# Performance work log

Hardware: AMD Instinct MI355X
Metric: run time of the kernel (lower is better)

The kernel has to match this reference:

```python
import jax, jax.numpy as jnp
import numpy as np

THRESHOLD = 1e-6
BLOCK_M = 64  # tile size over the batch/row dimension (prescan granularity)


def setup_inputs() -> dict:
    key = jax.random.key(0)
    k_x, k_w, k_b, k_m = jax.random.split(key, 4)
    N, C_IN, C_OUT = 16384, 4096, 4096
    n_tiles = N // BLOCK_M
    x = jax.random.normal(k_x, (N, C_IN), dtype=jnp.float32)
    # which is what the Dynamic-K prescan exploits
    tile_mask = (jax.random.uniform(k_m, (n_tiles, C_IN)) > 0.6).astype(jnp.float32)
    x = (x.reshape(n_tiles, BLOCK_M, C_IN) * tile_mask[:, None, :]).reshape(N, C_IN)
    weight = jax.random.normal(k_w, (C_OUT, C_IN), dtype=jnp.float32) * 0.02
    bias = jax.random.normal(k_b, (C_OUT,), dtype=jnp.float32) * 0.01
    return {"x": x, "weight": weight, "bias": bias}


def reference(x, weight, bias):
    # Tile-level Dynamic-K sparse linear: per tile of BLOCK_M rows, a channel c
    # is active iff max |x[tile, c]| > threshold; only active channels are
    # multiplied/accumulated. Equivalent math: zero inactive channels, then GEMM.
    N, C_IN = x.shape
    n_tiles = N // BLOCK_M
    xt = x.reshape(n_tiles, BLOCK_M, C_IN)
    active = (jnp.max(jnp.abs(xt), axis=1) > THRESHOLD)  # [n_tiles, C_IN]
    xm = xt * active[:, None, :].astype(x.dtype)
    # y[t,b,o] = sum_c xm[t,b,c] * weight[o,c]
    y = jnp.einsum('tbc,oc->tbo', xm, weight).reshape(N, weight.shape[0])
    return y + bias[None, :]
```

## Files before the change

### kernel.cpp

```cpp
#include <hip/hip_runtime.h>
#include <cstdint>

#define THR 1e-6f
#define N_ROWS 16384
#define CIN 4096
#define COUT 4096
#define TILES 256
#define KCAP 2048

typedef _Float16 f16x8 __attribute__((ext_vector_type(8)));
typedef float floatx4 __attribute__((ext_vector_type(4)));

static __device__ __forceinline__ unsigned short f16b(_Float16 h) {
  union { _Float16 f; unsigned short u; } c; c.f = h; return c.u;
}

static __device__ __forceinline__ void gl_lds16(const void* g, void* l) {
  __builtin_amdgcn_global_load_lds(
      (const __attribute__((address_space(1))) void*)g,
      (__attribute__((address_space(3))) void*)l, 16, 0, 0);
}

__global__ __launch_bounds__(256) void k_wsplit(const float* __restrict__ W,
                                                uint32_t* __restrict__ Wtp) {
  __shared__ float t[64][65];
  int c0 = (blockIdx.x & 63) << 6;
  int o0 = (blockIdx.x >> 6) << 6;
  int tid = threadIdx.x;
#pragma unroll
  for (int q = 0; q < 16; ++q) {
    int idx = q * 256 + tid;
    int ro = idx >> 6, ci = idx & 63;
    t[ci][ro] = W[(size_t)(o0 + ro) * CIN + c0 + ci];
  }
  __syncthreads();
#pragma unroll
  for (int q = 0; q < 16; ++q) {
    int idx = q * 256 + tid;
    int cr = idx >> 6, oi = idx & 63;
    float v = t[cr][oi];
    _Float16 h = (_Float16)v;
    _Float16 l = (_Float16)(v - (float)h);
    Wtp[(size_t)(c0 + cr) * COUT + o0 + oi] = ((uint32_t)f16b(h) << 16) | f16b(l);
  }
}

__global__ __launch_bounds__(256) void k_prescan(const float* __restrict__ x,
                                                 unsigned short* __restrict__ gidx,
                                                 int* __restrict__ cnts,
                                                 unsigned short* __restrict__ xch,
                                                 unsigned short* __restrict__ xcl) {
  int t = blockIdx.x;
  int tid = threadIdx.x;
  const float* xt = x + (size_t)t * 64 * CIN;

  float mx[16];
#pragma unroll
  for (int i = 0; i < 16; ++i) mx[i] = 0.f;
  for (int b = 0; b < 64; ++b) {
    const float4* row4 = (const float4*)(xt + (size_t)b * CIN);
#pragma unroll
    for (int j = 0; j < 4; ++j) {
      float4 v = row4[tid * 4 + j];
      mx[j * 4 + 0] = fmaxf(mx[j * 4 + 0], fabsf(v.x));
      mx[j * 4 + 1] = fmaxf(mx[j * 4 + 1], fabsf(v.y));
      mx[j * 4 + 2] = fmaxf(mx[j * 4 + 2], fabsf(v.z));
      mx[j * 4 + 3] = fmaxf(mx[j * 4 + 3], fabsf(v.w));
    }
  }
  int cnt = 0;
#pragma unroll
  for (int i = 0; i < 16; ++i) cnt += (mx[i] > THR) ? 1 : 0;

  __shared__ int scan[256];
  __shared__ unsigned short sidx[KCAP];
  scan[tid] = cnt;
  __syncthreads();
  for (int s = 1; s < 256; s <<= 1) {
    int v = (tid >= s) ? scan[tid - s] : 0;
    __syncthreads();
    scan[tid] += v;
    __syncthreads();
  }
  int pos = scan[tid] - cnt;
  int total = scan[255];
  int cntPad = (total + 63) & ~63;
  if (cntPad > KCAP) cntPad = KCAP;

#pragma unroll
  for (int i = 0; i < 16; ++i) {
    if (mx[i] > THR) {
      if (pos < KCAP) sidx[pos] = (unsigned short)(tid * 16 + i);
      ++pos;
    }
  }
  for (int k = total + tid; k < cntPad; k += 256) sidx[k] = 0;
  if (tid == 0) cnts[t] = cntPad;
  __syncthreads();

  for (int k = tid; k < cntPad; k += 256) gidx[t * KCAP + k] = sidx[k];

  for (int b = 0; b < 64; ++b) {
    const float* row = xt + (size_t)b * CIN;
    size_t obase = ((size_t)t * 64 + b) * KCAP;
    for (int k = tid; k < cntPad; k += 256) {
      float v = (k < total) ? row[sidx[k]] : 0.f;
      _Float16 h = (_Float16)v;
      _Float16 l = (_Float16)(v - (float)h);
      xch[obase + k] = f16b(h);
      xcl[obase + k] = f16b(l);
    }
  }
}

__global__ __launch_bounds__(256, 2) void k_gemm(const uint32_t* __restrict__ Wtp,
                                                 const unsigned short* __restrict__ gidx,
                                                 const int* __restrict__ cnts,
                                                 const unsigned short* __restrict__ xch,
                                                 const unsigned short* __restrict__ xcl,
                                                 const float* __restrict__ bias,
                                                 float* __restrict__ out) {
  __shared__ __attribute__((aligned(16))) char sA[16384];

  int bid = blockIdx.x + gridDim.x * blockIdx.y;
  int xcd = bid & 7;
  int i = bid >> 3;
  int t = i & 255;
  int o0 = ((xcd << 1) + (i >> 8)) << 8;

  int tid = threadIdx.x;
  int lane = tid & 63;
  int w = tid >> 6;
  int l15 = lane & 15, g = lane >> 4;
  int cntPad = cnts[t];

  floatx4 acc[4][4];
#pragma unroll
  for (int m = 0; m < 4; ++m)
#pragma unroll
    for (int n = 0; n < 4; ++n) acc[m][n] = (floatx4)0.f;

  int jx = ((lane & 7) * 16) ^ (((lane >> 3) & 7) << 4);
  int brow_s = lane >> 3;

  const int tKC = t * KCAP;

  for (int k0 = 0; k0 < cntPad; k0 += 64) {
    int cI[2][8];
#pragma unroll
    for (int ks = 0; ks < 2; ++ks)
#pragma unroll
      for (int q = 0; q < 8; ++q)
        cI[ks][q] = gidx[tKC + k0 + ks * 32 + g * 8 + q];

    __syncthreads();
#pragma unroll
    for (int q = 0; q < 4; ++q) {
      int ch = w + 4 * q;
      int plane = ch >> 3;
      int coff = (ch & 7) * 1024;
      int b = ((ch & 7) << 3) + brow_s;
      const unsigned short* srcp = plane ? xcl : xch;
      const char* gsrc = (const char*)(srcp + ((size_t)(t * 64 + b) * KCAP + k0)) + jx;
      gl_lds16(gsrc, sA + plane * 8192 + coff);
    }
    __syncthreads();

#pragma unroll
    for (int ks = 0; ks < 2; ++ks) {
      f16x8 Ah[4], Al[4];
#pragma unroll
      for (int m = 0; m < 4; ++m) {
        int b = m * 16 + l15;
        int off = (b * 128 + ks * 64 + g * 16) ^ ((b & 7) << 4);
        Ah[m] = *(const f16x8*)(sA + off);
        Al[m] = *(const f16x8*)(sA + 8192 + off);
      }
#pragma unroll
      for (int n = 0; n < 4; ++n) {
        int ocol = o0 + w * 64 + n * 16 + l15;
        uint32_t wv[8];
#pragma unroll
        for (int q = 0; q < 8; ++q)
          wv[q] = Wtp[(size_t)cI[ks][q] * COUT + ocol];
        union { f16x8 v; uint32_t u[4]; } Bh, Bl;
#pragma unroll
        for (int j = 0; j < 4; ++j) {
          Bh.u[j] = (wv[2 * j] >> 16) | (wv[2 * j + 1] & 0xFFFF0000u);
          Bl.u[j] = (wv[2 * j] & 0xFFFFu) | (wv[2 * j + 1] << 16);
        }
#pragma unroll
        for (int m = 0; m < 4; ++m) {
          acc[m][n] = __builtin_amdgcn_mfma_f32_16x16x32_f16(Ah[m], Bh.v, acc[m][n], 0, 0, 0);
          acc[m][n] = __builtin_amdgcn_mfma_f32_16x16x32_f16(Al[m], Bh.v, acc[m][n], 0, 0, 0);
          acc[m][n] = __builtin_amdgcn_mfma_f32_16x16x32_f16(Ah[m], Bl.v, acc[m][n], 0, 0, 0);
        }
      }
    }
  }

#pragma unroll
  for (int n = 0; n < 4; ++n) {
    int ocol = o0 + w * 64 + n * 16 + l15;
    float bv = bias[ocol];
#pragma unroll
    for (int m = 0; m < 4; ++m) {
      int row0 = t * 64 + m * 16 + g * 4;
#pragma unroll
      for (int r = 0; r < 4; ++r)
        out[(size_t)(row0 + r) * COUT + ocol] = acc[m][n][r] + bv;
    }
  }
}

__global__ __launch_bounds__(256) void k_dense_fallback(const float* __restrict__ x,
                                                        const float* __restrict__ W,
                                                        const float* __restrict__ bias,
                                                        float* __restrict__ out) {
  __shared__ float As[64][17];
  __shared__ float Bs[16][65];
  int r0 = blockIdx.y << 6, c0 = blockIdx.x << 6;
  int tid = threadIdx.x;
  int ty = tid >> 4, tx = tid & 15;
  float acc[4][4] = {};
  for (int k0 = 0; k0 < CIN; k0 += 16) {
    __syncthreads();
    {
      int bb = tid >> 2, kk = (tid & 3) * 4;
      float4 va = *(const float4*)&x[(size_t)(r0 + bb) * CIN + k0 + kk];
      As[bb][kk] = va.x; As[bb][kk + 1] = va.y; As[bb][kk + 2] = va.z; As[bb][kk + 3] = va.w;
      float4 vb = *(const float4*)&W[(size_t)(c0 + bb) * CIN + k0 + kk];
      Bs[kk][bb] = vb.x; Bs[kk + 1][bb] = vb.y; Bs[kk + 2][bb] = vb.z; Bs[kk + 3][bb] = vb.w;
    }
    __syncthreads();
#pragma unroll
    for (int kk = 0; kk < 16; ++kk) {
      float a[4], b[4];
#pragma unroll
      for (int q = 0; q < 4; ++q) a[q] = As[ty * 4 + q][kk];
#pragma unroll
      for (int j = 0; j < 4; ++j) b[j] = Bs[kk][tx * 4 + j];
#pragma unroll
      for (int q = 0; q < 4; ++q)
#pragma unroll
        for (int j = 0; j < 4; ++j) acc[q][j] += a[q] * b[j];
    }
  }
#pragma unroll
  for (int q = 0; q < 4; ++q) {
    int row = r0 + ty * 4 + q;
#pragma unroll
    for (int j = 0; j < 4; ++j) {
      int col = c0 + tx * 4 + j;
      out[(size_t)row * COUT + col] = acc[q][j] + bias[col];
    }
  }
}

extern "C" void kernel_launch(void* const* d_in, const int* in_sizes, int n_in,
                              void* d_out, int out_size, void* d_ws, size_t ws_size,
                              hipStream_t stream) {
  (void)in_sizes; (void)n_in; (void)out_size;
  const float* x = (const float*)d_in[0];
  const float* W = (const float*)d_in[1];
  const float* bias = (const float*)d_in[2];
  float* out = (float*)d_out;

  size_t offWtp = 0;
  size_t offXch = offWtp + (size_t)CIN * COUT * 4;
  size_t offXcl = offXch + (size_t)N_ROWS * KCAP * 2;
  size_t offIdx = offXcl + (size_t)N_ROWS * KCAP * 2;
  size_t offCnt = offIdx + (size_t)TILES * KCAP * 2;
  size_t need = offCnt + (size_t)TILES * 4;

  if (ws_size < need) {
    dim3 g(COUT / 64, N_ROWS / 64);
    k_dense_fallback<<<g, 256, 0, stream>>>(x, W, bias, out);
    return;
  }

  char* ws = (char*)d_ws;
  uint32_t* Wtp = (uint32_t*)(ws + offWtp);
  unsigned short* xch = (unsigned short*)(ws + offXch);
  unsigned short* xcl = (unsigned short*)(ws + offXcl);
  unsigned short* gidx = (unsigned short*)(ws + offIdx);
  int* cnts = (int*)(ws + offCnt);

  k_wsplit<<<dim3(64 * 64), 256, 0, stream>>>(W, Wtp);
  k_prescan<<<dim3(TILES), 256, 0, stream>>>(x, gidx, cnts, xch, xcl);
  k_gemm<<<dim3(COUT / 256, TILES), 256, 0, stream>>>(Wtp, gidx, cnts, xch, xcl, bias, out);
}
```

Before: 1.397 ms.

## Split prescan into colmax/scan/compact kernels and double-buffer GEMM LDS staging

The single 256-block prescan kernel becomes three kernels. A column-max kernel over 1024 blocks builds per-tile channel flags, a scan kernel turns them into compacted indices and per-channel positions, and a compaction kernel over 2048 blocks reads rows coalesced and scatters the split fp16 hi/lo values. The aim is to spread the memory-bound prescan across more of the GPU. The GEMM now double-buffers the LDS tile loads so the next k-chunk's global-to-LDS copy overlaps the current MFMA work. It also uses v_perm to unpack the weights and raises wave priority around the MFMAs. In exchange the workspace grows, there are extra launches and intermediate buffers, and the compaction does scattered stores.

```diff
diff --git a/kernel.cpp b/kernel.cpp
--- a/kernel.cpp
+++ b/kernel.cpp
@@ -45,70 +45,100 @@
   }
 }
 
-__global__ __launch_bounds__(256) void k_prescan(const float* __restrict__ x,
-                                                 unsigned short* __restrict__ gidx,
-                                                 int* __restrict__ cnts,
-                                                 unsigned short* __restrict__ xch,
-                                                 unsigned short* __restrict__ xcl) {
-  int t = blockIdx.x;
-  int tid = threadIdx.x;
+__global__ __launch_bounds__(256) void k_colmax(const float* __restrict__ x,
+                                                unsigned char* __restrict__ flags) {
+  int t = blockIdx.x >> 2;
+  int q = blockIdx.x & 3;
+  int c = (q << 10) + threadIdx.x * 4;
   const float* xt = x + (size_t)t * 64 * CIN;
-
-  float mx[16];
-#pragma unroll
-  for (int i = 0; i < 16; ++i) mx[i] = 0.f;
+  float4 m = {0.f, 0.f, 0.f, 0.f};
   for (int b = 0; b < 64; ++b) {
-    const float4* row4 = (const float4*)(xt + (size_t)b * CIN);
-#pragma unroll
-    for (int j = 0; j < 4; ++j) {
-      float4 v = row4[tid * 4 + j];
-      mx[j * 4 + 0] = fmaxf(mx[j * 4 + 0], fabsf(v.x));
-      mx[j * 4 + 1] = fmaxf(mx[j * 4 + 1], fabsf(v.y));
-      mx[j * 4 + 2] = fmaxf(mx[j * 4 + 2], fabsf(v.z));
-      mx[j * 4 + 3] = fmaxf(mx[j * 4 + 3], fabsf(v.w));
-    }
-  }
-  int cnt = 0;
-#pragma unroll
-  for (int i = 0; i < 16; ++i) cnt += (mx[i] > THR) ? 1 : 0;
-
+    float4 v = *(const float4*)(xt + (size_t)b * CIN + c);
+    m.x = fmaxf(m.x, fabsf(v.x));
+    m.y = fmaxf(m.y, fabsf(v.y));
+    m.z = fmaxf(m.z, fabsf(v.z));
+    m.w = fmaxf(m.w, fabsf(v.w));
+  }
+  uchar4 fl;
+  fl.x = m.x > THR; fl.y = m.y > THR; fl.z = m.z > THR; fl.w = m.w > THR;
+  *(uchar4*)&flags[(size_t)t * CIN + c] = fl;
+}
+
+__global__ __launch_bounds__(256) void k_scan(const unsigned char* __restrict__ flags,
+                                              unsigned short* __restrict__ gidx,
+                                              int* __restrict__ cnts,
+                                              int* __restrict__ tots,
+                                              unsigned short* __restrict__ ppos) {
+  int t = blockIdx.x, tid = threadIdx.x;
+  const unsigned char* f = flags + (size_t)t * CIN;
+  uint4 v = *(const uint4*)(f + tid * 16);
+  int cnt = (int)((v.x * 0x01010101u) >> 24) + (int)((v.y * 0x01010101u) >> 24) +
+            (int)((v.z * 0x01010101u) >> 24) + (int)((v.w * 0x01010101u) >> 24);
   __shared__ int scan[256];
-  __shared__ unsigned short sidx[KCAP];
   scan[tid] = cnt;
   __syncthreads();
   for (int s = 1; s < 256; s <<= 1) {
-    int v = (tid >= s) ? scan[tid - s] : 0;
+    int u = (tid >= s) ? scan[tid - s] : 0;
     __syncthreads();
-    scan[tid] += v;
+    scan[tid] += u;
     __syncthreads();
   }
   int pos = scan[tid] - cnt;
   int total = scan[255];
   int cntPad = (total + 63) & ~63;
   if (cntPad > KCAP) cntPad = KCAP;
-
+  unsigned char bs[16];
+  *(uint4*)bs = v;
 #pragma unroll
   for (int i = 0; i < 16; ++i) {
-    if (mx[i] > THR) {
-      if (pos < KCAP) sidx[pos] = (unsigned short)(tid * 16 + i);
+    int c = tid * 16 + i;
+    if (bs[i]) {
+      if (pos < KCAP) {
+        gidx[t * KCAP + pos] = (unsigned short)c;
+        ppos[(size_t)t * CIN + c] = (unsigned short)pos;
+      } else {
+        ppos[(size_t)t * CIN + c] = 0xFFFF;
+      }
       ++pos;
-    }
-  }
-  for (int k = total + tid; k < cntPad; k += 256) sidx[k] = 0;
-  if (tid == 0) cnts[t] = cntPad;
-  __syncthreads();
-
-  for (int k = tid; k < cntPad; k += 256) gidx[t * KCAP + k] = sidx[k];
-
-  for (int b = 0; b < 64; ++b) {
-    const float* row = xt + (size_t)b * CIN;
-    size_t obase = ((size_t)t * 64 + b) * KCAP;
-    for (int k = tid; k < cntPad; k += 256) {
-      float v = (k < total) ? row[sidx[k]] : 0.f;
-      _Float16 h = (_Float16)v;
-      _Float16 l = (_Float16)(v - (float)h);
-      xch[obase + k] = f16b(h);
-      xcl[obase + k] = f16b(l);
+    } else {
+      ppos[(size_t)t * CIN + c] = 0xFFFF;
+    }
+  }
+  for (int k = total + tid; k < cntPad; k += 256) gidx[t * KCAP + k] = 0;
+  if (tid == 0) { cnts[t] = cntPad; tots[t] = total; }
+}
+
+__global__ __launch_bounds__(256) void k_compact(const float* __restrict__ x,
+                                                 const unsigned short* __restrict__ ppos,
+                                                 const int* __restrict__ cnts,
+                                                 const int* __restrict__ tots,
+                                                 unsigned short* __restrict__ xch,
+                                                 unsigned short* __restrict__ xcl) {
+  int t = blockIdx.x >> 3;
+  int rg = blockIdx.x & 7;
+  int tid = threadIdx.x;
+  int cntPad = cnts[t];
+  int total = tots[t];
+  const unsigned short* pp = ppos + (size_t)t * CIN;
+  for (int r = rg * 8; r < rg * 8 + 8; ++r) {
+    int row = t * 64 + r;
+    const float4* xr = (const float4*)(x + (size_t)row * CIN);
+    size_t ob = (size_t)row * KCAP;
+    for (int k = total + tid; k < cntPad; k += 256) { xch[ob + k] = 0; xcl[ob + k] = 0; }
+    for (int j = tid; j < CIN / 4; j += 256) {
+      float4 v = xr[j];
+      ushort4 p = *(const ushort4*)(pp + j * 4);
+      float vv[4] = {v.x, v.y, v.z, v.w};
+      unsigned short ps[4] = {p.x, p.y, p.z, p.w};
+#pragma unroll
+      for (int e = 0; e < 4; ++e) {
+        if (ps[e] != 0xFFFF) {
+          _Float16 h = (_Float16)vv[e];
+          _Float16 l = (_Float16)(vv[e] - (float)h);
+          xch[ob + ps[e]] = f16b(h);
+          xcl[ob + ps[e]] = f16b(l);
+        }
+      }
     }
   }
 }
@@ -120,7 +150,7 @@
                                                  const unsigned short* __restrict__ xcl,
                                                  const float* __restrict__ bias,
                                                  float* __restrict__ out) {
-  __shared__ __attribute__((aligned(16))) char sA[16384];
+  __shared__ __attribute__((aligned(16))) char sA[2][16384];
 
   int bid = blockIdx.x + gridDim.x * blockIdx.y;
   int xcd = bid & 7;
@@ -133,6 +163,7 @@
   int w = tid >> 6;
   int l15 = lane & 15, g = lane >> 4;
   int cntPad = cnts[t];
+  int nt = cntPad >> 6;
 
   floatx4 acc[4][4];
 #pragma unroll
@@ -142,18 +173,9 @@
 
   int jx = ((lane & 7) * 16) ^ (((lane >> 3) & 7) << 4);
   int brow_s = lane >> 3;
-
   const int tKC = t * KCAP;
 
-  for (int k0 = 0; k0 < cntPad; k0 += 64) {
-    int cI[2][8];
-#pragma unroll
-    for (int ks = 0; ks < 2; ++ks)
-#pragma unroll
-      for (int q = 0; q < 8; ++q)
-        cI[ks][q] = gidx[tKC + k0 + ks * 32 + g * 8 + q];
-
-    __syncthreads();
+  auto STAGE = [&](int buf, int kk) {
 #pragma unroll
     for (int q = 0; q < 4; ++q) {
       int ch = w + 4 * q;
@@ -161,11 +183,29 @@
       int coff = (ch & 7) * 1024;
       int b = ((ch & 7) << 3) + brow_s;
       const unsigned short* srcp = plane ? xcl : xch;
-      const char* gsrc = (const char*)(srcp + ((size_t)(t * 64 + b) * KCAP + k0)) + jx;
-      gl_lds16(gsrc, sA + plane * 8192 + coff);
-    }
-    __syncthreads();
-
+      const char* gsrc = (const char*)(srcp + ((size_t)(t * 64 + b) * KCAP + kk)) + jx;
+      gl_lds16(gsrc, &sA[buf][plane * 8192 + coff]);
+    }
+  };
+
+  if (nt > 0) STAGE(0, 0);
+  asm volatile("s_waitcnt vmcnt(0)" ::: "memory");
+  __builtin_amdgcn_s_barrier();
+
+  for (int it = 0; it < nt; ++it) {
+    int cur = it & 1;
+    int k0 = it << 6;
+
+    int cI[2][8];
+#pragma unroll
+    for (int ks = 0; ks < 2; ++ks)
+#pragma unroll
+      for (int q = 0; q < 8; ++q)
+        cI[ks][q] = gidx[tKC + k0 + ks * 32 + g * 8 + q];
+
+    if (it + 1 < nt) STAGE(cur ^ 1, k0 + 64);
+
+    const char* sbase = sA[cur];
 #pragma unroll
     for (int ks = 0; ks < 2; ++ks) {
       f16x8 Ah[4], Al[4];
@@ -173,8 +213,8 @@
       for (int m = 0; m < 4; ++m) {
         int b = m * 16 + l15;
         int off = (b * 128 + ks * 64 + g * 16) ^ ((b & 7) << 4);
-        Ah[m] = *(const f16x8*)(sA + off);
-        Al[m] = *(const f16x8*)(sA + 8192 + off);
+        Ah[m] = *(const f16x8*)(sbase + off);
+        Al[m] = *(const f16x8*)(sbase + 8192 + off);
       }
 #pragma unroll
       for (int n = 0; n < 4; ++n) {
@@ -182,21 +222,26 @@
         uint32_t wv[8];
 #pragma unroll
         for (int q = 0; q < 8; ++q)
-          wv[q] = Wtp[(size_t)cI[ks][q] * COUT + ocol];
+          wv[q] = Wtp[((unsigned)cI[ks][q] << 12) + (unsigned)ocol];
         union { f16x8 v; uint32_t u[4]; } Bh, Bl;
 #pragma unroll
         for (int j = 0; j < 4; ++j) {
-          Bh.u[j] = (wv[2 * j] >> 16) | (wv[2 * j + 1] & 0xFFFF0000u);
-          Bl.u[j] = (wv[2 * j] & 0xFFFFu) | (wv[2 * j + 1] << 16);
+          Bh.u[j] = __builtin_amdgcn_perm(wv[2 * j + 1], wv[2 * j], 0x07060302u);
+          Bl.u[j] = __builtin_amdgcn_perm(wv[2 * j + 1], wv[2 * j], 0x05040100u);
         }
+        __builtin_amdgcn_s_setprio(1);
 #pragma unroll
         for (int m = 0; m < 4; ++m) {
           acc[m][n] = __builtin_amdgcn_mfma_f32_16x16x32_f16(Ah[m], Bh.v, acc[m][n], 0, 0, 0);
           acc[m][n] = __builtin_amdgcn_mfma_f32_16x16x32_f16(Al[m], Bh.v, acc[m][n], 0, 0, 0);
           acc[m][n] = __builtin_amdgcn_mfma_f32_16x16x32_f16(Ah[m], Bl.v, acc[m][n], 0, 0, 0);
         }
+        __builtin_amdgcn_s_setprio(0);
       }
     }
+
+    asm volatile("s_waitcnt vmcnt(0)" ::: "memory");
+    __builtin_amdgcn_s_barrier();
   }
 
 #pragma unroll
@@ -270,8 +315,11 @@
   size_t offXch = offWtp + (size_t)CIN * COUT * 4;
   size_t offXcl = offXch + (size_t)N_ROWS * KCAP * 2;
   size_t offIdx = offXcl + (size_t)N_ROWS * KCAP * 2;
-  size_t offCnt = offIdx + (size_t)TILES * KCAP * 2;
-  size_t need = offCnt + (size_t)TILES * 4;
+  size_t offPpos = offIdx + (size_t)TILES * KCAP * 2;
+  size_t offFlag = offPpos + (size_t)TILES * CIN * 2;
+  size_t offCnt = offFlag + (size_t)TILES * CIN;
+  size_t offTot = offCnt + 4096;
+  size_t need = offTot + 4096;
 
   if (ws_size < need) {
     dim3 g(COUT / 64, N_ROWS / 64);
@@ -284,9 +332,14 @@
   unsigned short* xch = (unsigned short*)(ws + offXch);
   unsigned short* xcl = (unsigned short*)(ws + offXcl);
   unsigned short* gidx = (unsigned short*)(ws + offIdx);
+  unsigned short* ppos = (unsigned short*)(ws + offPpos);
+  unsigned char* flags = (unsigned char*)(ws + offFlag);
   int* cnts = (int*)(ws + offCnt);
+  int* tots = (int*)(ws + offTot);
 
   k_wsplit<<<dim3(64 * 64), 256, 0, stream>>>(W, Wtp);
-  k_prescan<<<dim3(TILES), 256, 0, stream>>>(x, gidx, cnts, xch, xcl);
+  k_colmax<<<dim3(TILES * 4), 256, 0, stream>>>(x, flags);
+  k_scan<<<dim3(TILES), 256, 0, stream>>>(flags, gidx, cnts, tots, ppos);
+  k_compact<<<dim3(TILES * 8), 256, 0, stream>>>(x, ppos, cnts, tots, xch, xcl);
   k_gemm<<<dim3(COUT / 256, TILES), 256, 0, stream>>>(Wtp, gidx, cnts, xch, xcl, bias, out);
 }
```

Result: faster. 1.286 ms (-8.0%).
